# Optimization experiments

Measured on AMD Instinct MI355X. Metric: run time of the kernel, lower is better.

The kernel has to match this reference:

```python
import jax, jax.numpy as jnp
import numpy as np

TEMPERATURE = 0.5  # init kwarg; forward's temperature arg is unused in the original

def _l2norm(x, eps=1e-12):
    # matches F.normalize(dim=-1)
    n = jnp.sqrt(jnp.sum(x * x, axis=-1, keepdims=True))
    return x / jnp.maximum(n, eps)

def setup_inputs() -> dict:
    key = jax.random.key(0)
    k1, k2 = jax.random.split(key)
    h1 = jax.random.normal(k1, (8192, 128), dtype=jnp.float32)
    h2 = jax.random.normal(k2, (8192, 128), dtype=jnp.float32)
    return {"h1": h1, "h2": h2}

def reference(h1, h2):
    t = TEMPERATURE
    h1n = _l2norm(h1)
    h2n = _l2norm(h2)
    h = jnp.concatenate([h1n, h2n], axis=0)              # [2N, d]
    sim = jnp.exp(jnp.matmul(h, h.T) / t)                # [2N, 2N]
    # masked_select of off-diagonal then row-sum == full row-sum minus diagonal
    denom = jnp.sum(sim, axis=-1) - jnp.diagonal(sim)    # [2N]
    pos = jnp.exp(jnp.sum(h1n * h2n, axis=-1) / t)       # [N]
    pos = jnp.concatenate([pos, pos], axis=0)            # [2N]
    loss = -jnp.log(pos / denom)
    return jnp.mean(loss)
```

## Files before the change

### kernel.cpp

```cpp
#include <hip/hip_runtime.h>
#include <hip/hip_bf16.h>

#define N_ROWS 8192
#define DIM    128
#define TWO_N  16384
#define NBLK   64
#define NTRI   (NBLK * (NBLK + 1) / 2)
#define EXP_TWO 7.38905609893065f
#define H_SCALE 1.6986436f

typedef __attribute__((ext_vector_type(8))) short short8;
typedef __attribute__((ext_vector_type(4))) float float4v;

__device__ inline void async_copy16(const void* g, void* l) {
  __builtin_amdgcn_global_load_lds(
      (const __attribute__((address_space(1))) void*)g,
      (__attribute__((address_space(3))) void*)l, 16, 0, 0);
}

__device__ inline float fast_exp2(float x) {
#if __has_builtin(__builtin_amdgcn_exp2f)
  return __builtin_amdgcn_exp2f(x);
#else
  return exp2f(x);
#endif
}


__global__ __launch_bounds__(256) void norm_kernel(
    const float* __restrict__ h1, const float* __restrict__ h2,
    __hip_bfloat16* __restrict__ Hb, float* __restrict__ posdot,
    float* __restrict__ rowsum) {
  if (threadIdx.x < 8) rowsum[blockIdx.x * 8 + threadIdx.x] = 0.0f;

  int lane = threadIdx.x & 63;
  int w    = threadIdx.x >> 6;
  int row  = blockIdx.x * 4 + w;

  const float2* p1 = (const float2*)(h1 + (size_t)row * DIM);
  const float2* p2 = (const float2*)(h2 + (size_t)row * DIM);
  float2 v1 = p1[lane];
  float2 v2 = p2[lane];

  float ss1 = v1.x * v1.x + v1.y * v1.y;
  float ss2 = v2.x * v2.x + v2.y * v2.y;
  #pragma unroll
  for (int s = 32; s; s >>= 1) {
    ss1 += __shfl_xor(ss1, s);
    ss2 += __shfl_xor(ss2, s);
  }
  float inv1 = 1.0f / fmaxf(sqrtf(ss1), 1e-12f);
  float inv2 = 1.0f / fmaxf(sqrtf(ss2), 1e-12f);

  float ax = v1.x * inv1, ay = v1.y * inv1;
  float bx = v2.x * inv2, by = v2.y * inv2;

  float pd = ax * bx + ay * by;
  #pragma unroll
  for (int s = 32; s; s >>= 1) pd += __shfl_xor(pd, s);

  int Kt = lane >> 4, q8 = (lane & 15) >> 2, sic = (lane & 3) * 2;
  short* Hs = (short*)Hb;
  {
    int r1 = row;
    size_t off = (size_t)((r1 >> 4) * 4 + Kt) * 512 + (q8 * 16 + (r1 & 15)) * 8 + sic;
    __hip_bfloat162 t;
    t.x = __float2bfloat16(ax * H_SCALE); t.y = __float2bfloat16(ay * H_SCALE);
    *(__hip_bfloat162*)(Hs + off) = t;
  }
  {
    int r2 = row + N_ROWS;
    size_t off = (size_t)((r2 >> 4) * 4 + Kt) * 512 + (q8 * 16 + (r2 & 15)) * 8 + sic;
    __hip_bfloat162 t;
    t.x = __float2bfloat16(bx * H_SCALE); t.y = __float2bfloat16(by * H_SCALE);
    *(__hip_bfloat162*)(Hs + off) = t;
  }

  if (lane == 0) posdot[row] = pd;
}

__global__ __launch_bounds__(512, 2) void ntx_main(
    const __hip_bfloat16* __restrict__ Hb, float* __restrict__ rowsum) {
  __shared__ short smem[32768];
  __shared__ float colacc[8][256];
  const short* H = (const short*)Hb;

  int tid  = threadIdx.x;
  int lane = tid & 63;
  int w    = tid >> 6;
  int q    = lane >> 4;
  int m    = lane & 15;

  int t0 = blockIdx.x;
  int I = (int)((129.0f - sqrtf(129.0f * 129.0f - 8.0f * (float)t0)) * 0.5f);
  while ((I + 1) * (129 - (I + 1)) / 2 <= t0) ++I;
  while (I * (129 - I) / 2 > t0) --I;
  int J = I + (t0 - I * (129 - I) / 2);
  bool diag = (I == J);

  int rowbase = I * 256 + w * 32;

  const short* gpanel = H + (size_t)J * 32768;
  #pragma unroll
  for (int it = 0; it < 8; ++it)
    async_copy16(gpanel + it * 4096 + tid * 8, (void*)&smem[it * 4096 + tid * 8]);

  short8 a[2][4];
  #pragma unroll
  for (int r = 0; r < 2; ++r)
    #pragma unroll
    for (int s = 0; s < 4; ++s)
      a[r][s] = *(const short8*)(H + (size_t)((I * 16 + w * 2 + r) * 4 + s) * 512 + lane * 8);
  #pragma unroll
  for (int r = 0; r < 2; ++r)
    #pragma unroll
    for (int s = 0; s < 4; ++s)
      asm volatile("" : "+v"(a[r][s]));

  float rowacc[2][4];
  #pragma unroll
  for (int r = 0; r < 2; ++r)
    #pragma unroll
    for (int i = 0; i < 4; ++i) rowacc[r][i] = 0.0f;

  __syncthreads();

  #pragma unroll 4
  for (int cs = 0; cs < 16; ++cs) {
    short8 b[4];
    #pragma unroll
    for (int s = 0; s < 4; ++s)
      b[s] = *(const short8*)&smem[cs * 2048 + s * 512 + lane * 8];
    float cp = 0.0f;
    #pragma unroll
    for (int r = 0; r < 2; ++r) {
      float4v acc = {0.f, 0.f, 0.f, 0.f};
      #pragma unroll
      for (int s = 0; s < 4; ++s)
        acc = __builtin_amdgcn_mfma_f32_16x16x32_bf16(a[r][s], b[s], acc, 0, 0, 0);
      #pragma unroll
      for (int i = 0; i < 4; ++i) {
        float e = fast_exp2(acc[i]);
        rowacc[r][i] += e;
        cp += e;
      }
    }
    if (!diag) {
      cp += __shfl_xor(cp, 16);
      cp += __shfl_xor(cp, 32);
      if (q == 0) colacc[w][cs * 16 + m] = cp;
    }
  }

  #pragma unroll
  for (int r = 0; r < 2; ++r)
    #pragma unroll
    for (int i = 0; i < 4; ++i) {
      float v = rowacc[r][i];
      v += __shfl_xor(v, 1);
      v += __shfl_xor(v, 2);
      v += __shfl_xor(v, 4);
      v += __shfl_xor(v, 8);
      rowacc[r][i] = v;
    }
  if (m == 0) {
    #pragma unroll
    for (int r = 0; r < 2; ++r)
      #pragma unroll
      for (int i = 0; i < 4; ++i)
        atomicAdd(&rowsum[rowbase + r * 16 + q * 4 + i], rowacc[r][i]);
  }

  if (!diag) {
    __syncthreads();
    if (tid < 256) {
      float v = 0.0f;
      #pragma unroll
      for (int ww = 0; ww < 8; ++ww) v += colacc[ww][tid];
      atomicAdd(&rowsum[J * 256 + tid], v);
    }
  }
}

__global__ __launch_bounds__(1024) void finalize(
    const float* __restrict__ rowsum, const float* __restrict__ posdot,
    float* __restrict__ out) {
  __shared__ float red[32];
  int tid = threadIdx.x;
  const float4* rs4 = (const float4*)rowsum;
  const float4* pd4 = (const float4*)posdot;
  float ld = 0.0f, pp = 0.0f;
  #pragma unroll
  for (int it = 0; it < 4; ++it) {
    float4 v = rs4[tid + it * 1024];
    ld += logf(v.x - EXP_TWO) + logf(v.y - EXP_TWO) +
          logf(v.z - EXP_TWO) + logf(v.w - EXP_TWO);
  }
  #pragma unroll
  for (int it = 0; it < 2; ++it) {
    float4 v = pd4[tid + it * 1024];
    pp += v.x + v.y + v.z + v.w;
  }
  #pragma unroll
  for (int s = 32; s; s >>= 1) {
    ld += __shfl_xor(ld, s);
    pp += __shfl_xor(pp, s);
  }
  if ((tid & 63) == 0) {
    red[tid >> 6] = ld;
    red[16 + (tid >> 6)] = pp;
  }
  __syncthreads();
  if (tid == 0) {
    float tl = 0.0f, tp = 0.0f;
    #pragma unroll
    for (int i = 0; i < 16; ++i) { tl += red[i]; tp += red[16 + i]; }
    *out = (tl - 4.0f * tp) / (float)TWO_N;
  }
}

extern "C" void kernel_launch(void* const* d_in, const int* in_sizes, int n_in,
                              void* d_out, int out_size, void* d_ws, size_t ws_size,
                              hipStream_t stream) {
  const float* h1 = (const float*)d_in[0];
  const float* h2 = (const float*)d_in[1];
  char* ws = (char*)d_ws;

  __hip_bfloat16* Hb = (__hip_bfloat16*)ws;
  float* rowsum      = (float*)(ws + 4194304);
  float* posdot      = (float*)(ws + 4194304 + 65536);
  float* out         = (float*)d_out;

  norm_kernel<<<N_ROWS / 4, 256, 0, stream>>>(h1, h2, Hb, posdot, rowsum);
  ntx_main<<<NTRI, 512, 0, stream>>>(Hb, rowsum);
  finalize<<<1, 1024, 0, stream>>>(rowsum, posdot, out);
}
```

Before: 116.4 us.

## Switch main tile to 32x32x16 MFMA with 4-wave blocks and matching layout

Replaces the 16x16x32 bf16 MFMA with the 32x32x16 variant and changes the packed bf16 layout written by the norm kernel to fit its operand format. The main kernel now uses 256 threads, with each wave covering 64 rows as two 32-row tiles. This gives more math per operand load and fewer LDS reads and shuffles per output element. The cost is more accumulator registers (2x16 row sums plus a 16-wide accumulator), which may reduce occupancy.

```diff
diff --git a/kernel.cpp b/kernel.cpp
--- a/kernel.cpp
+++ b/kernel.cpp
@@ -10,7 +10,7 @@
 #define H_SCALE 1.6986436f
 
 typedef __attribute__((ext_vector_type(8))) short short8;
-typedef __attribute__((ext_vector_type(4))) float float4v;
+typedef __attribute__((ext_vector_type(16))) float float16v;
 
 __device__ inline void async_copy16(const void* g, void* l) {
   __builtin_amdgcn_global_load_lds(
@@ -59,18 +59,18 @@
   #pragma unroll
   for (int s = 32; s; s >>= 1) pd += __shfl_xor(pd, s);
 
-  int Kt = lane >> 4, q8 = (lane & 15) >> 2, sic = (lane & 3) * 2;
+  int Kt = lane >> 3, kh = (lane >> 2) & 1, sic = (2 * lane) & 7;
   short* Hs = (short*)Hb;
   {
     int r1 = row;
-    size_t off = (size_t)((r1 >> 4) * 4 + Kt) * 512 + (q8 * 16 + (r1 & 15)) * 8 + sic;
+    size_t off = (size_t)((r1 >> 5) * 8 + Kt) * 512 + (kh * 32 + (r1 & 31)) * 8 + sic;
     __hip_bfloat162 t;
     t.x = __float2bfloat16(ax * H_SCALE); t.y = __float2bfloat16(ay * H_SCALE);
     *(__hip_bfloat162*)(Hs + off) = t;
   }
   {
     int r2 = row + N_ROWS;
-    size_t off = (size_t)((r2 >> 4) * 4 + Kt) * 512 + (q8 * 16 + (r2 & 15)) * 8 + sic;
+    size_t off = (size_t)((r2 >> 5) * 8 + Kt) * 512 + (kh * 32 + (r2 & 31)) * 8 + sic;
     __hip_bfloat162 t;
     t.x = __float2bfloat16(bx * H_SCALE); t.y = __float2bfloat16(by * H_SCALE);
     *(__hip_bfloat162*)(Hs + off) = t;
@@ -79,17 +79,17 @@
   if (lane == 0) posdot[row] = pd;
 }
 
-__global__ __launch_bounds__(512, 2) void ntx_main(
+__global__ __launch_bounds__(256, 2) void ntx_main(
     const __hip_bfloat16* __restrict__ Hb, float* __restrict__ rowsum) {
   __shared__ short smem[32768];
-  __shared__ float colacc[8][256];
+  __shared__ float colacc[4][256];
   const short* H = (const short*)Hb;
 
   int tid  = threadIdx.x;
   int lane = tid & 63;
   int w    = tid >> 6;
-  int q    = lane >> 4;
-  int m    = lane & 15;
+  int hi   = lane >> 5;
+  int c31  = lane & 31;
 
   int t0 = blockIdx.x;
   int I = (int)((129.0f - sqrtf(129.0f * 129.0f - 8.0f * (float)t0)) * 0.5f);
@@ -98,87 +98,83 @@
   int J = I + (t0 - I * (129 - I) / 2);
   bool diag = (I == J);
 
-  int rowbase = I * 256 + w * 32;
-
   const short* gpanel = H + (size_t)J * 32768;
   #pragma unroll
-  for (int it = 0; it < 8; ++it)
-    async_copy16(gpanel + it * 4096 + tid * 8, (void*)&smem[it * 4096 + tid * 8]);
-
-  short8 a[2][4];
-  #pragma unroll
-  for (int r = 0; r < 2; ++r)
-    #pragma unroll
-    for (int s = 0; s < 4; ++s)
-      a[r][s] = *(const short8*)(H + (size_t)((I * 16 + w * 2 + r) * 4 + s) * 512 + lane * 8);
-  #pragma unroll
-  for (int r = 0; r < 2; ++r)
-    #pragma unroll
-    for (int s = 0; s < 4; ++s)
+  for (int it = 0; it < 16; ++it)
+    async_copy16(gpanel + it * 2048 + tid * 8, (void*)&smem[it * 2048 + tid * 8]);
+
+  short8 a[2][8];
+  #pragma unroll
+  for (int r = 0; r < 2; ++r)
+    #pragma unroll
+    for (int s = 0; s < 8; ++s)
+      a[r][s] = *(const short8*)(H + (size_t)((I * 8 + w * 2 + r) * 8 + s) * 512 + lane * 8);
+  #pragma unroll
+  for (int r = 0; r < 2; ++r)
+    #pragma unroll
+    for (int s = 0; s < 8; ++s)
       asm volatile("" : "+v"(a[r][s]));
 
-  float rowacc[2][4];
-  #pragma unroll
-  for (int r = 0; r < 2; ++r)
-    #pragma unroll
-    for (int i = 0; i < 4; ++i) rowacc[r][i] = 0.0f;
+  float rowacc[2][16];
+  #pragma unroll
+  for (int r = 0; r < 2; ++r)
+    #pragma unroll
+    for (int i = 0; i < 16; ++i) rowacc[r][i] = 0.0f;
 
   __syncthreads();
 
-  #pragma unroll 4
-  for (int cs = 0; cs < 16; ++cs) {
-    short8 b[4];
-    #pragma unroll
-    for (int s = 0; s < 4; ++s)
-      b[s] = *(const short8*)&smem[cs * 2048 + s * 512 + lane * 8];
+  #pragma unroll 2
+  for (int j = 0; j < 8; ++j) {
+    short8 b[8];
+    #pragma unroll
+    for (int s = 0; s < 8; ++s)
+      b[s] = *(const short8*)&smem[(j * 8 + s) * 512 + lane * 8];
     float cp = 0.0f;
     #pragma unroll
     for (int r = 0; r < 2; ++r) {
-      float4v acc = {0.f, 0.f, 0.f, 0.f};
+      float16v acc = {};
       #pragma unroll
-      for (int s = 0; s < 4; ++s)
-        acc = __builtin_amdgcn_mfma_f32_16x16x32_bf16(a[r][s], b[s], acc, 0, 0, 0);
+      for (int s = 0; s < 8; ++s)
+        acc = __builtin_amdgcn_mfma_f32_32x32x16_bf16(a[r][s], b[s], acc, 0, 0, 0);
       #pragma unroll
-      for (int i = 0; i < 4; ++i) {
+      for (int i = 0; i < 16; ++i) {
         float e = fast_exp2(acc[i]);
         rowacc[r][i] += e;
         cp += e;
       }
     }
     if (!diag) {
-      cp += __shfl_xor(cp, 16);
       cp += __shfl_xor(cp, 32);
-      if (q == 0) colacc[w][cs * 16 + m] = cp;
+      if (hi == 0) colacc[w][j * 32 + c31] = cp;
     }
   }
 
-  #pragma unroll
-  for (int r = 0; r < 2; ++r)
-    #pragma unroll
-    for (int i = 0; i < 4; ++i) {
+  int rowbase = I * 256 + w * 64;
+  #pragma unroll
+  for (int r = 0; r < 2; ++r)
+    #pragma unroll
+    for (int i = 0; i < 16; ++i) {
       float v = rowacc[r][i];
       v += __shfl_xor(v, 1);
       v += __shfl_xor(v, 2);
       v += __shfl_xor(v, 4);
       v += __shfl_xor(v, 8);
+      v += __shfl_xor(v, 16);
       rowacc[r][i] = v;
     }
-  if (m == 0) {
+  if (c31 == 0) {
     #pragma unroll
     for (int r = 0; r < 2; ++r)
       #pragma unroll
-      for (int i = 0; i < 4; ++i)
-        atomicAdd(&rowsum[rowbase + r * 16 + q * 4 + i], rowacc[r][i]);
+      for (int i = 0; i < 16; ++i)
+        atomicAdd(&rowsum[rowbase + r * 32 + (i & 3) + 8 * (i >> 2) + 4 * hi],
+                  rowacc[r][i]);
   }
 
   if (!diag) {
     __syncthreads();
-    if (tid < 256) {
-      float v = 0.0f;
-      #pragma unroll
-      for (int ww = 0; ww < 8; ++ww) v += colacc[ww][tid];
-      atomicAdd(&rowsum[J * 256 + tid], v);
-    }
+    float v = colacc[0][tid] + colacc[1][tid] + colacc[2][tid] + colacc[3][tid];
+    atomicAdd(&rowsum[J * 256 + tid], v);
   }
 }
 
@@ -232,6 +228,6 @@
   float* out         = (float*)d_out;
 
   norm_kernel<<<N_ROWS / 4, 256, 0, stream>>>(h1, h2, Hb, posdot, rowsum);
-  ntx_main<<<NTRI, 512, 0, stream>>>(Hb, rowsum);
+  ntx_main<<<NTRI, 256, 0, stream>>>(Hb, rowsum);
   finalize<<<1, 1024, 0, stream>>>(rowsum, posdot, out);
 }
```

After: 137.8 us. 18.4% more time.
